# Kernel optimization log

Measured on AMD Instinct MI355X. Metric: run time of the kernel, lower is better.

The kernel has to match this reference:

```python
import jax, jax.numpy as jnp
import numpy as np

HIDDEN = 1024
HEADS = 16
HEAD_DIM = HIDDEN // HEADS
B, S = 2, 2048


def setup_inputs() -> dict:
    key = jax.random.key(0)
    k1, k2, k3 = jax.random.split(key, 3)
    x = jax.random.normal(k1, (B, S, HIDDEN), dtype=jnp.float32)
    qkv_w = jax.random.normal(k2, (3 * HIDDEN, HIDDEN), dtype=jnp.float32) * (HIDDEN ** -0.5)
    out_w = jax.random.normal(k3, (HIDDEN, HIDDEN), dtype=jnp.float32) * (HIDDEN ** -0.5)
    return {"x": x, "qkv_w": qkv_w, "out_w": out_w}


def reference(x, qkv_w, out_w):
    b, s, d = x.shape
    scale = HEAD_DIM ** -0.5
    # qkv projection (Linear without bias: x @ W^T)
    qkv = x @ qkv_w.T                                   # [b, s, 3d]
    qkv = qkv.reshape(b, s, 3, HEADS, HEAD_DIM)
    qkv = jnp.transpose(qkv, (2, 0, 3, 1, 4))           # [3, b, h, s, hd]
    q, k, v = qkv[0] * scale, qkv[1], qkv[2]
    # causal attention (blocked torch loop == full causal softmax attention)
    scores = jnp.einsum('bhqd,bhkd->bhqk', q, k)        # [b, h, s, s]
    causal = jnp.tril(jnp.ones((s, s), dtype=bool))
    scores = jnp.where(causal[None, None], scores, -jnp.inf)
    weights = jax.nn.softmax(scores, axis=-1)
    attn = jnp.einsum('bhqk,bhkd->bhqd', weights, v)    # [b, h, s, hd]
    attn = jnp.transpose(attn, (0, 2, 1, 3)).reshape(b, s, d)
    return attn @ out_w.T
```

## Files before the change

kernel.cpp:

```cpp
#include <hip/hip_runtime.h>
#include <hip/hip_bf16.h>
#include <math.h>

#define HIDDEN 1024
#define HEADS 16
#define HDIM 64
#define BATCH 2
#define SEQ 2048
#define BHN (BATCH*HEADS)
#define MTOT (BATCH*SEQ)

typedef __attribute__((ext_vector_type(8))) short short8;
typedef __attribute__((ext_vector_type(4))) float floatx4;

#define GL2LDS(gsrc, ldst) __builtin_amdgcn_global_load_lds( \
    (const __attribute__((address_space(1))) void*)(gsrc), \
    (__attribute__((address_space(3))) void*)(ldst), 16, 0, 0)

__device__ __forceinline__ short f2bf(float f) {
  union { float f; unsigned u; } v; v.f = f;
  unsigned u = v.u;
  unsigned r = (u + 0x7fffu + ((u >> 16) & 1u)) >> 16;
  return (short)r;
}

__global__ __launch_bounds__(256) void cvt3_f32_bf16(
    const float* __restrict__ a, const float* __restrict__ b, const float* __restrict__ c,
    short* __restrict__ oa, short* __restrict__ ob, short* __restrict__ oc) {
  int i = blockIdx.x * 256 + threadIdx.x;
  const float* src; short* dst; int j;
  if (i < 1048576)      { src = a; dst = oa; j = i; }
  else if (i < 1835008) { src = b; dst = ob; j = i - 1048576; }
  else                  { src = c; dst = oc; j = i - 1835008; }
  float4 f = reinterpret_cast<const float4*>(src)[j];
  short4 o;
  o.x = f2bf(f.x); o.y = f2bf(f.y); o.z = f2bf(f.z); o.w = f2bf(f.w);
  reinterpret_cast<short4*>(dst)[j] = o;
}

template<int EPI>
__global__ __launch_bounds__(256) void gemm_bt(
    const short* __restrict__ A, const short* __restrict__ B,
    int M, int N, int K,
    float* __restrict__ outF,
    short* __restrict__ outQ, short* __restrict__ outK, short* __restrict__ outV)
{
  __shared__ __align__(16) short As[128*32];
  __shared__ __align__(16) short Bs[128*32];
  const int tid = threadIdx.x;
  const int wv = tid >> 6;
  const int lane = tid & 63;
  const int l15 = lane & 15;
  const int quad = lane >> 4;
  const int wm = wv >> 1, wn = wv & 1;
  const int row0 = blockIdx.y * 128, col0 = blockIdx.x * 128;

  floatx4 acc[4][4];
#pragma unroll
  for (int i = 0; i < 4; i++)
#pragma unroll
    for (int j = 0; j < 4; j++) acc[i][j] = (floatx4){0.f, 0.f, 0.f, 0.f};

  for (int k0 = 0; k0 < K; k0 += 32) {
#pragma unroll
    for (int rd = 0; rd < 2; ++rd) {
      int chunk = rd * 256 + tid;
      int r = chunk >> 2, c = (chunk & 3) << 3;
      GL2LDS(A + (long)(row0 + r) * K + k0 + c, As + (rd * 256 + wv * 64) * 8);
    }
#pragma unroll
    for (int rd = 0; rd < 2; ++rd) {
      int chunk = rd * 256 + tid;
      int r = chunk >> 2, c = (chunk & 3) << 3;
      GL2LDS(B + (long)(col0 + r) * K + k0 + c, Bs + (rd * 256 + wv * 64) * 8);
    }
    __syncthreads();

    short8 af[4], bfr[4];
#pragma unroll
    for (int mi = 0; mi < 4; mi++)
      af[mi] = *(const short8*)(As + (wm * 64 + mi * 16 + l15) * 32 + quad * 8);
#pragma unroll
    for (int ni = 0; ni < 4; ni++)
      bfr[ni] = *(const short8*)(Bs + (wn * 64 + ni * 16 + l15) * 32 + quad * 8);
#pragma unroll
    for (int mi = 0; mi < 4; mi++)
#pragma unroll
      for (int ni = 0; ni < 4; ni++)
        acc[mi][ni] = __builtin_amdgcn_mfma_f32_16x16x32_bf16(af[mi], bfr[ni], acc[mi][ni], 0, 0, 0);
    __syncthreads();
  }

  if (EPI == 2) {
#pragma unroll
    for (int mi = 0; mi < 4; mi++) {
      int rr = row0 + wm * 64 + mi * 16 + quad * 4;
#pragma unroll
      for (int ni = 0; ni < 4; ni++) {
        int cc = col0 + wn * 64 + ni * 16 + l15;
#pragma unroll
        for (int r = 0; r < 4; r++)
          outF[(long)(rr + r) * N + cc] = acc[mi][ni][r];
      }
    }
  } else {
#pragma unroll
    for (int mi = 0; mi < 4; mi++) {
      int rowg = row0 + wm * 64 + mi * 16 + quad * 4;
#pragma unroll
      for (int ni = 0; ni < 4; ni++) {
        int j = col0 + wn * 64 + ni * 16 + l15;
        int t = j >> 10;
        int rem = j & 1023;
        int h = rem >> 6, d = rem & 63;
#pragma unroll
        for (int r = 0; r < 4; r++) {
          int i = rowg + r;
          int b = i >> 11, s = i & 2047;
          int bh = b * HEADS + h;
          float v = acc[mi][ni][r];
          if (t == 0)      outQ[(bh * SEQ + s) * HDIM + d] = f2bf(v * 0.18033688011112042f);
          else if (t == 1) outK[(bh * SEQ + s) * HDIM + d] = f2bf(v);
          else             outV[(bh * HDIM + d) * SEQ + s] = f2bf(v);
        }
      }
    }
  }
}

__device__ __forceinline__ void stage_kv(const short* __restrict__ kg,
                                         const short* __restrict__ vT,
                                         int bh, int kt, short* KsB, short* VsB,
                                         int tid, int wv) {
#pragma unroll
  for (int i = 0; i < 2; ++i) {
    int slot = i * 256 + tid;
    int r = slot >> 3;
    int sc = ((slot & 7) ^ (r & 7)) << 3;
    GL2LDS(kg + (bh * SEQ + kt * 64 + r) * HDIM + sc, KsB + (i * 256 + wv * 64) * 8);
    GL2LDS(vT + (bh * HDIM + r) * SEQ + kt * 64 + sc, VsB + (i * 256 + wv * 64) * 8);
  }
}

__global__ __launch_bounds__(256) void flash_attn(
    const short* __restrict__ q, const short* __restrict__ kg,
    const short* __restrict__ vT, short* __restrict__ attn)
{
  __shared__ __align__(16) short Ks[2][64 * 64];
  __shared__ __align__(16) short Vs[2][64 * 64];
  __shared__ __align__(16) short Ps[4][32 * 64];

  const int tid = threadIdx.x;
  const int wv = tid >> 6, lane = tid & 63;
  const int l15 = lane & 15, quad = lane >> 4;
  const int bh = blockIdx.y;
  const int t = (bh < 16) ? (15 - (int)blockIdx.x) : (int)blockIdx.x;
  const int m0 = t * 128 + wv * 32;
  const int swl = l15 & 7;

  short8 aq[2][2];
#pragma unroll
  for (int mi = 0; mi < 2; mi++) {
    const short* qp = q + (bh * SEQ + m0 + mi * 16 + l15) * HDIM + quad * 8;
    aq[mi][0] = *(const short8*)(qp);
    aq[mi][1] = *(const short8*)(qp + 32);
  }

  const short ONE = (short)0x3F80;
  const short8 ones = {ONE, ONE, ONE, ONE, ONE, ONE, ONE, ONE};

  floatx4 o[2][4], lsum[2];
#pragma unroll
  for (int mi = 0; mi < 2; mi++) {
    lsum[mi] = (floatx4){0.f, 0.f, 0.f, 0.f};
#pragma unroll
    for (int nt = 0; nt < 4; nt++) o[mi][nt] = (floatx4){0.f, 0.f, 0.f, 0.f};
  }

  const int ntiles = 2 * t + 2;
  stage_kv(kg, vT, bh, 0, Ks[0], Vs[0], tid, wv);

  for (int kt = 0; kt < ntiles; ++kt) {
    __syncthreads();
    const int buf = kt & 1;
    if (kt + 1 < ntiles)
      stage_kv(kg, vT, bh, kt + 1, Ks[buf ^ 1], Vs[buf ^ 1], tid, wv);

    if (kt * 64 <= m0 + 31) {
      const short* KsB = Ks[buf];
      const short* VsB = Vs[buf];

      short8 bk[4][2];
#pragma unroll
      for (int nh = 0; nh < 4; nh++)
#pragma unroll
        for (int kk = 0; kk < 2; kk++)
          bk[nh][kk] = *(const short8*)(KsB + (nh * 16 + l15) * 64 + (((kk * 4 + quad) ^ swl) << 3));
      floatx4 scf[2][4];
#pragma unroll
      for (int mi = 0; mi < 2; mi++)
#pragma unroll
        for (int nh = 0; nh < 4; nh++) scf[mi][nh] = (floatx4){0.f, 0.f, 0.f, 0.f};
#pragma unroll
      for (int mi = 0; mi < 2; mi++)
#pragma unroll
        for (int nh = 0; nh < 4; nh++)
#pragma unroll
          for (int kk = 0; kk < 2; kk++)
            scf[mi][nh] = __builtin_amdgcn_mfma_f32_16x16x32_bf16(aq[mi][kk], bk[nh][kk], scf[mi][nh], 0, 0, 0);

      const bool full = (kt * 64 + 63) <= m0;
      short* Pw = Ps[wv];
#pragma unroll
      for (int mi = 0; mi < 2; mi++)
#pragma unroll
        for (int nh = 0; nh < 4; nh++)
#pragma unroll
          for (int r = 0; r < 4; r++) {
            float p = __builtin_amdgcn_exp2f(scf[mi][nh][r]);
            if (!full) {
              const int col = kt * 64 + nh * 16 + l15;
              const int qrow = m0 + mi * 16 + quad * 4 + r;
              p = (col <= qrow) ? p : 0.f;
            }
            const unsigned u = __builtin_bit_cast(unsigned, p);
            const int pr = mi * 16 + quad * 4 + r;
            const int ch = (nh * 2 + (l15 >> 3)) ^ (pr & 7);
            Pw[pr * 64 + (ch << 3) + (l15 & 7)] = (short)(u >> 16);
          }

      __asm__ volatile("s_waitcnt lgkmcnt(0)" ::: "memory");

      short8 bv[4][2];
#pragma unroll
      for (int nt = 0; nt < 4; nt++)
#pragma unroll
        for (int kk = 0; kk < 2; kk++)
          bv[nt][kk] = *(const short8*)(VsB + (nt * 16 + l15) * 64 + (((kk * 4 + quad) ^ swl) << 3));
      short8 pa[2][2];
#pragma unroll
      for (int mi = 0; mi < 2; mi++)
#pragma unroll
        for (int kk = 0; kk < 2; kk++)
          pa[mi][kk] = *(const short8*)(Pw + (mi * 16 + l15) * 64 + (((kk * 4 + quad) ^ swl) << 3));
#pragma unroll
      for (int mi = 0; mi < 2; mi++)
#pragma unroll
        for (int kk = 0; kk < 2; kk++)
          lsum[mi] = __builtin_amdgcn_mfma_f32_16x16x32_bf16(pa[mi][kk], ones, lsum[mi], 0, 0, 0);
#pragma unroll
      for (int mi = 0; mi < 2; mi++)
#pragma unroll
        for (int nt = 0; nt < 4; nt++)
#pragma unroll
          for (int kk = 0; kk < 2; kk++)
            o[mi][nt] = __builtin_amdgcn_mfma_f32_16x16x32_bf16(pa[mi][kk], bv[nt][kk], o[mi][nt], 0, 0, 0);
    }
  }

  const int b = bh >> 4, h = bh & 15;
#pragma unroll
  for (int mi = 0; mi < 2; mi++)
#pragma unroll
    for (int r = 0; r < 4; r++) {
      const float inv = 1.0f / lsum[mi][r];
      const int s = m0 + mi * 16 + quad * 4 + r;
#pragma unroll
      for (int nt = 0; nt < 4; nt++)
        attn[(b * SEQ + s) * HIDDEN + h * HDIM + nt * 16 + l15] = f2bf(o[mi][nt][r] * inv);
    }
}

extern "C" void kernel_launch(void* const* d_in, const int* in_sizes, int n_in,
                              void* d_out, int out_size, void* d_ws, size_t ws_size,
                              hipStream_t stream) {
  const float* x     = (const float*)d_in[0];
  const float* qkv_w = (const float*)d_in[1];
  const float* out_w = (const float*)d_in[2];
  float* out = (float*)d_out;

  short* xb   = (short*)d_ws;
  short* wqb  = xb  + MTOT * HIDDEN;
  short* wob  = wqb + 3 * HIDDEN * HIDDEN;
  short* qB   = wob + HIDDEN * HIDDEN;
  short* kB   = qB  + BHN * SEQ * HDIM;
  short* vTB  = kB  + BHN * SEQ * HDIM;
  short* attn = vTB + BHN * SEQ * HDIM;

  cvt3_f32_bf16<<<dim3(8192), dim3(256), 0, stream>>>(x, qkv_w, out_w, xb, wqb, wob);

  gemm_bt<1><<<dim3(3 * HIDDEN / 128, MTOT / 128), dim3(256), 0, stream>>>(
      xb, wqb, MTOT, 3 * HIDDEN, HIDDEN, nullptr, qB, kB, vTB);

  flash_attn<<<dim3(SEQ / 128, BHN), dim3(256), 0, stream>>>(qB, kB, vTB, attn);

  gemm_bt<2><<<dim3(HIDDEN / 128, MTOT / 128), dim3(256), 0, stream>>>(
      attn, wob, MTOT, HIDDEN, HIDDEN, out, nullptr, nullptr, nullptr);
}
```

Measured before the change: 210.6 us.

## Pair long/short causal query tiles per block and load K/V directly to registers

The attention kernel now gives each block two 64-row query tiles, one from the long end and one from the short end of the causal triangle, so every block does equal work. K/V fragments are read straight from global memory into registers instead of being double-buffered through LDS, which removes the block-wide barriers. Scores are computed transposed (K times Q), so P can be packed and written to LDS with 64-bit stores. The output-projection GEMM is templated on tile width and uses 64-column tiles to launch more blocks. The risks are redundant global K/V loads across the four waves, with L2 reuse only, and lower MFMA density in the narrower GEMM tile.

```diff
diff --git a/kernel.cpp b/kernel.cpp
--- a/kernel.cpp
+++ b/kernel.cpp
@@ -38,28 +38,30 @@
   reinterpret_cast<short4*>(dst)[j] = o;
 }
 
-template<int EPI>
+template<int EPI, int BN>
 __global__ __launch_bounds__(256) void gemm_bt(
     const short* __restrict__ A, const short* __restrict__ B,
     int M, int N, int K,
     float* __restrict__ outF,
     short* __restrict__ outQ, short* __restrict__ outK, short* __restrict__ outV)
 {
+  constexpr int WN = BN / 2;
+  constexpr int NI = BN / 32;
   __shared__ __align__(16) short As[128*32];
-  __shared__ __align__(16) short Bs[128*32];
+  __shared__ __align__(16) short Bs[BN*32];
   const int tid = threadIdx.x;
   const int wv = tid >> 6;
   const int lane = tid & 63;
   const int l15 = lane & 15;
   const int quad = lane >> 4;
   const int wm = wv >> 1, wn = wv & 1;
-  const int row0 = blockIdx.y * 128, col0 = blockIdx.x * 128;
-
-  floatx4 acc[4][4];
+  const int row0 = blockIdx.y * 128, col0 = blockIdx.x * BN;
+
+  floatx4 acc[4][NI];
 #pragma unroll
   for (int i = 0; i < 4; i++)
 #pragma unroll
-    for (int j = 0; j < 4; j++) acc[i][j] = (floatx4){0.f, 0.f, 0.f, 0.f};
+    for (int j = 0; j < NI; j++) acc[i][j] = (floatx4){0.f, 0.f, 0.f, 0.f};
 
   for (int k0 = 0; k0 < K; k0 += 32) {
 #pragma unroll
@@ -69,24 +71,24 @@
       GL2LDS(A + (long)(row0 + r) * K + k0 + c, As + (rd * 256 + wv * 64) * 8);
     }
 #pragma unroll
-    for (int rd = 0; rd < 2; ++rd) {
+    for (int rd = 0; rd < BN / 64; ++rd) {
       int chunk = rd * 256 + tid;
       int r = chunk >> 2, c = (chunk & 3) << 3;
       GL2LDS(B + (long)(col0 + r) * K + k0 + c, Bs + (rd * 256 + wv * 64) * 8);
     }
     __syncthreads();
 
-    short8 af[4], bfr[4];
+    short8 af[4], bfr[NI];
 #pragma unroll
     for (int mi = 0; mi < 4; mi++)
       af[mi] = *(const short8*)(As + (wm * 64 + mi * 16 + l15) * 32 + quad * 8);
 #pragma unroll
-    for (int ni = 0; ni < 4; ni++)
-      bfr[ni] = *(const short8*)(Bs + (wn * 64 + ni * 16 + l15) * 32 + quad * 8);
+    for (int ni = 0; ni < NI; ni++)
+      bfr[ni] = *(const short8*)(Bs + (wn * WN + ni * 16 + l15) * 32 + quad * 8);
 #pragma unroll
     for (int mi = 0; mi < 4; mi++)
 #pragma unroll
-      for (int ni = 0; ni < 4; ni++)
+      for (int ni = 0; ni < NI; ni++)
         acc[mi][ni] = __builtin_amdgcn_mfma_f32_16x16x32_bf16(af[mi], bfr[ni], acc[mi][ni], 0, 0, 0);
     __syncthreads();
   }
@@ -96,8 +98,8 @@
     for (int mi = 0; mi < 4; mi++) {
       int rr = row0 + wm * 64 + mi * 16 + quad * 4;
 #pragma unroll
-      for (int ni = 0; ni < 4; ni++) {
-        int cc = col0 + wn * 64 + ni * 16 + l15;
+      for (int ni = 0; ni < NI; ni++) {
+        int cc = col0 + wn * WN + ni * 16 + l15;
 #pragma unroll
         for (int r = 0; r < 4; r++)
           outF[(long)(rr + r) * N + cc] = acc[mi][ni][r];
@@ -108,8 +110,8 @@
     for (int mi = 0; mi < 4; mi++) {
       int rowg = row0 + wm * 64 + mi * 16 + quad * 4;
 #pragma unroll
-      for (int ni = 0; ni < 4; ni++) {
-        int j = col0 + wn * 64 + ni * 16 + l15;
+      for (int ni = 0; ni < NI; ni++) {
+        int j = col0 + wn * WN + ni * 16 + l15;
         int t = j >> 10;
         int rem = j & 1023;
         int h = rem >> 6, d = rem & 63;
@@ -128,41 +130,28 @@
   }
 }
 
-__device__ __forceinline__ void stage_kv(const short* __restrict__ kg,
-                                         const short* __restrict__ vT,
-                                         int bh, int kt, short* KsB, short* VsB,
-                                         int tid, int wv) {
-#pragma unroll
-  for (int i = 0; i < 2; ++i) {
-    int slot = i * 256 + tid;
-    int r = slot >> 3;
-    int sc = ((slot & 7) ^ (r & 7)) << 3;
-    GL2LDS(kg + (bh * SEQ + kt * 64 + r) * HDIM + sc, KsB + (i * 256 + wv * 64) * 8);
-    GL2LDS(vT + (bh * HDIM + r) * SEQ + kt * 64 + sc, VsB + (i * 256 + wv * 64) * 8);
-  }
-}
-
-__global__ __launch_bounds__(256) void flash_attn(
-    const short* __restrict__ q, const short* __restrict__ kg,
+__global__ __launch_bounds__(256, 2) void flash_attn(
+    const short* __restrict__ qg, const short* __restrict__ kg,
     const short* __restrict__ vT, short* __restrict__ attn)
 {
-  __shared__ __align__(16) short Ks[2][64 * 64];
-  __shared__ __align__(16) short Vs[2][64 * 64];
   __shared__ __align__(16) short Ps[4][32 * 64];
-
   const int tid = threadIdx.x;
   const int wv = tid >> 6, lane = tid & 63;
   const int l15 = lane & 15, quad = lane >> 4;
-  const int bh = blockIdx.y;
-  const int t = (bh < 16) ? (15 - (int)blockIdx.x) : (int)blockIdx.x;
-  const int m0 = t * 128 + wv * 32;
+  const int bh = blockIdx.x;
+  const int p  = blockIdx.y;
+  const int tL = 31 - p, tS = p;
+  int m0[2];
+  m0[0] = tL * 64 + wv * 16;
+  m0[1] = tS * 64 + wv * 16;
   const int swl = l15 & 7;
+  short* Pw = &Ps[wv][0];
 
   short8 aq[2][2];
 #pragma unroll
   for (int mi = 0; mi < 2; mi++) {
-    const short* qp = q + (bh * SEQ + m0 + mi * 16 + l15) * HDIM + quad * 8;
-    aq[mi][0] = *(const short8*)(qp);
+    const short* qp = qg + (long)(bh * SEQ + m0[mi] + l15) * HDIM + quad * 8;
+    aq[mi][0] = *(const short8*)qp;
     aq[mi][1] = *(const short8*)(qp + 32);
   }
 
@@ -177,84 +166,56 @@
     for (int nt = 0; nt < 4; nt++) o[mi][nt] = (floatx4){0.f, 0.f, 0.f, 0.f};
   }
 
-  const int ntiles = 2 * t + 2;
-  stage_kv(kg, vT, bh, 0, Ks[0], Vs[0], tid, wv);
-
-  for (int kt = 0; kt < ntiles; ++kt) {
-    __syncthreads();
-    const int buf = kt & 1;
-    if (kt + 1 < ntiles)
-      stage_kv(kg, vT, bh, kt + 1, Ks[buf ^ 1], Vs[buf ^ 1], tid, wv);
-
-    if (kt * 64 <= m0 + 31) {
-      const short* KsB = Ks[buf];
-      const short* VsB = Vs[buf];
-
-      short8 bk[4][2];
-#pragma unroll
-      for (int nh = 0; nh < 4; nh++)
-#pragma unroll
-        for (int kk = 0; kk < 2; kk++)
-          bk[nh][kk] = *(const short8*)(KsB + (nh * 16 + l15) * 64 + (((kk * 4 + quad) ^ swl) << 3));
-      floatx4 scf[2][4];
-#pragma unroll
-      for (int mi = 0; mi < 2; mi++)
-#pragma unroll
-        for (int nh = 0; nh < 4; nh++) scf[mi][nh] = (floatx4){0.f, 0.f, 0.f, 0.f};
-#pragma unroll
-      for (int mi = 0; mi < 2; mi++)
-#pragma unroll
-        for (int nh = 0; nh < 4; nh++)
-#pragma unroll
-          for (int kk = 0; kk < 2; kk++)
-            scf[mi][nh] = __builtin_amdgcn_mfma_f32_16x16x32_bf16(aq[mi][kk], bk[nh][kk], scf[mi][nh], 0, 0, 0);
-
-      const bool full = (kt * 64 + 63) <= m0;
-      short* Pw = Ps[wv];
-#pragma unroll
-      for (int mi = 0; mi < 2; mi++)
-#pragma unroll
-        for (int nh = 0; nh < 4; nh++)
-#pragma unroll
-          for (int r = 0; r < 4; r++) {
-            float p = __builtin_amdgcn_exp2f(scf[mi][nh][r]);
-            if (!full) {
-              const int col = kt * 64 + nh * 16 + l15;
-              const int qrow = m0 + mi * 16 + quad * 4 + r;
-              p = (col <= qrow) ? p : 0.f;
-            }
-            const unsigned u = __builtin_bit_cast(unsigned, p);
-            const int pr = mi * 16 + quad * 4 + r;
-            const int ch = (nh * 2 + (l15 >> 3)) ^ (pr & 7);
-            Pw[pr * 64 + (ch << 3) + (l15 & 7)] = (short)(u >> 16);
+  for (int kt = 0; kt <= tL; ++kt) {
+    short8 kf[4][2], vf[4][2];
+#pragma unroll
+    for (int nh = 0; nh < 4; nh++) {
+      const short* kp = kg + (long)(bh * SEQ + kt * 64 + nh * 16 + l15) * HDIM + quad * 8;
+      kf[nh][0] = *(const short8*)kp;
+      kf[nh][1] = *(const short8*)(kp + 32);
+      const short* vp = vT + (long)(bh * HDIM + nh * 16 + l15) * SEQ + kt * 64 + quad * 8;
+      vf[nh][0] = *(const short8*)vp;
+      vf[nh][1] = *(const short8*)(vp + 32);
+    }
+
+    const int nmi = (kt <= tS) ? 2 : 1;
+    for (int mi = 0; mi < nmi; ++mi) {
+      const int tmi = (mi == 0) ? tL : tS;
+      const bool partial = (kt == tmi);
+      const int qrow = m0[mi] + l15;
+
+#pragma unroll
+      for (int nh = 0; nh < 4; nh++) {
+        floatx4 sc = (floatx4){0.f, 0.f, 0.f, 0.f};
+        sc = __builtin_amdgcn_mfma_f32_16x16x32_bf16(kf[nh][0], aq[mi][0], sc, 0, 0, 0);
+        sc = __builtin_amdgcn_mfma_f32_16x16x32_bf16(kf[nh][1], aq[mi][1], sc, 0, 0, 0);
+        unsigned u[4];
+#pragma unroll
+        for (int r = 0; r < 4; r++) {
+          float pe = __builtin_amdgcn_exp2f(sc[r]);
+          if (partial) {
+            const int kpos = kt * 64 + nh * 16 + quad * 4 + r;
+            pe = (kpos <= qrow) ? pe : 0.f;
           }
-
+          u[r] = __builtin_bit_cast(unsigned, pe) & 0xffff0000u;
+        }
+        uint2 wpk;
+        wpk.x = (u[0] >> 16) | u[1];
+        wpk.y = (u[2] >> 16) | u[3];
+        *(uint2*)(Pw + (mi * 16 + l15) * 64 +
+                  ((((nh << 1) + (quad >> 1)) ^ swl) << 3) + ((quad & 1) << 2)) = wpk;
+      }
       __asm__ volatile("s_waitcnt lgkmcnt(0)" ::: "memory");
-
-      short8 bv[4][2];
-#pragma unroll
-      for (int nt = 0; nt < 4; nt++)
-#pragma unroll
-        for (int kk = 0; kk < 2; kk++)
-          bv[nt][kk] = *(const short8*)(VsB + (nt * 16 + l15) * 64 + (((kk * 4 + quad) ^ swl) << 3));
-      short8 pa[2][2];
-#pragma unroll
-      for (int mi = 0; mi < 2; mi++)
-#pragma unroll
-        for (int kk = 0; kk < 2; kk++)
-          pa[mi][kk] = *(const short8*)(Pw + (mi * 16 + l15) * 64 + (((kk * 4 + quad) ^ swl) << 3));
-#pragma unroll
-      for (int mi = 0; mi < 2; mi++)
-#pragma unroll
-        for (int kk = 0; kk < 2; kk++)
-          lsum[mi] = __builtin_amdgcn_mfma_f32_16x16x32_bf16(pa[mi][kk], ones, lsum[mi], 0, 0, 0);
-#pragma unroll
-      for (int mi = 0; mi < 2; mi++)
-#pragma unroll
-        for (int nt = 0; nt < 4; nt++)
-#pragma unroll
-          for (int kk = 0; kk < 2; kk++)
-            o[mi][nt] = __builtin_amdgcn_mfma_f32_16x16x32_bf16(pa[mi][kk], bv[nt][kk], o[mi][nt], 0, 0, 0);
+      const short* pr = Pw + (mi * 16 + l15) * 64;
+      short8 pa0 = *(const short8*)(pr + (((0 + quad) ^ swl) << 3));
+      short8 pa1 = *(const short8*)(pr + (((4 + quad) ^ swl) << 3));
+      lsum[mi] = __builtin_amdgcn_mfma_f32_16x16x32_bf16(pa0, ones, lsum[mi], 0, 0, 0);
+      lsum[mi] = __builtin_amdgcn_mfma_f32_16x16x32_bf16(pa1, ones, lsum[mi], 0, 0, 0);
+#pragma unroll
+      for (int nt = 0; nt < 4; nt++) {
+        o[mi][nt] = __builtin_amdgcn_mfma_f32_16x16x32_bf16(pa0, vf[nt][0], o[mi][nt], 0, 0, 0);
+        o[mi][nt] = __builtin_amdgcn_mfma_f32_16x16x32_bf16(pa1, vf[nt][1], o[mi][nt], 0, 0, 0);
+      }
     }
   }
 
@@ -264,10 +225,10 @@
 #pragma unroll
     for (int r = 0; r < 4; r++) {
       const float inv = 1.0f / lsum[mi][r];
-      const int s = m0 + mi * 16 + quad * 4 + r;
+      const int s = m0[mi] + quad * 4 + r;
 #pragma unroll
       for (int nt = 0; nt < 4; nt++)
-        attn[(b * SEQ + s) * HIDDEN + h * HDIM + nt * 16 + l15] = f2bf(o[mi][nt][r] * inv);
+        attn[(long)(b * SEQ + s) * HIDDEN + h * HDIM + nt * 16 + l15] = f2bf(o[mi][nt][r] * inv);
     }
 }
 
@@ -289,11 +250,11 @@
 
   cvt3_f32_bf16<<<dim3(8192), dim3(256), 0, stream>>>(x, qkv_w, out_w, xb, wqb, wob);
 
-  gemm_bt<1><<<dim3(3 * HIDDEN / 128, MTOT / 128), dim3(256), 0, stream>>>(
+  gemm_bt<1, 128><<<dim3(3 * HIDDEN / 128, MTOT / 128), dim3(256), 0, stream>>>(
       xb, wqb, MTOT, 3 * HIDDEN, HIDDEN, nullptr, qB, kB, vTB);
 
-  flash_attn<<<dim3(SEQ / 128, BHN), dim3(256), 0, stream>>>(qB, kB, vTB, attn);
-
-  gemm_bt<2><<<dim3(HIDDEN / 128, MTOT / 128), dim3(256), 0, stream>>>(
+  flash_attn<<<dim3(BHN, 16), dim3(256), 0, stream>>>(qB, kB, vTB, attn);
+
+  gemm_bt<2, 64><<<dim3(HIDDEN / 64, MTOT / 128), dim3(256), 0, stream>>>(
       attn, wob, MTOT, HIDDEN, HIDDEN, out, nullptr, nullptr, nullptr);
 }
```

Result: slower. 247.3 us (+17.4%).
